# Optimization experiments

Hardware: AMD Instinct MI355X
Metric: run time of the kernel (lower is better)

The kernel has to match this reference:

```python
import jax, jax.numpy as jnp
import numpy as np

N_QUBITS = 10
DIM = 1 << N_QUBITS  # 1024

# Constant QFT matrix (PennyLane convention: F[j,k] = w^{jk}/sqrt(N), w = exp(2*pi*i/N),
# wire 0 = most significant bit). Symmetric, so state @ F == F @ state per sample.
_jk = (np.outer(np.arange(DIM), np.arange(DIM)) % DIM).astype(np.float64)
QFT_MAT = jnp.asarray((np.exp(2j * np.pi * _jk / DIM) / np.sqrt(DIM)).astype(np.complex64))


def _apply_1q(state, U, q):
    """Apply 2x2 gate U to wire q (wire 0 = MSB). state: [B, DIM] complex."""
    B = state.shape[0]
    left, right = 1 << q, 1 << (N_QUBITS - 1 - q)
    s = state.reshape(B, left, 2, right)
    s = jnp.einsum('ij,bajc->baic', U, s)
    return s.reshape(B, DIM)


def _apply_cnot(state, c, t):
    """CNOT with control c, target t (wire 0 = MSB)."""
    B = state.shape[0]
    a, b = (c, t) if c < t else (t, c)
    s = state.reshape(B, 1 << a, 2, 1 << (b - a - 1), 2, 1 << (N_QUBITS - 1 - b))
    ctrl_ax, tgt_ax = (2, 4) if c < t else (4, 2)
    s0 = jax.lax.index_in_dim(s, 0, ctrl_ax, keepdims=False)
    s1 = jax.lax.index_in_dim(s, 1, ctrl_ax, keepdims=False)
    ta = tgt_ax - 1 if tgt_ax > ctrl_ax else tgt_ax  # target axis after squeezing ctrl
    s1 = jnp.flip(s1, axis=ta)  # X on target when control == 1
    s = jnp.stack([s0, s1], axis=ctrl_ax)
    return s.reshape(B, DIM)


def _rx(t):
    c = jnp.cos(t / 2).astype(jnp.complex64)
    s = (-1j * jnp.sin(t / 2)).astype(jnp.complex64)
    return jnp.stack([jnp.stack([c, s]), jnp.stack([s, c])])


def _ry(t):
    c = jnp.cos(t / 2).astype(jnp.complex64)
    s = jnp.sin(t / 2).astype(jnp.complex64)
    return jnp.stack([jnp.stack([c, -s]), jnp.stack([s, c])])


def _rz(t):
    e = jnp.exp(-0.5j * t.astype(jnp.complex64))
    z = jnp.zeros((), jnp.complex64)
    return jnp.stack([jnp.stack([e, z]), jnp.stack([z, jnp.conj(e)])])


def _forward(x, weights):
    B = x.shape[0]
    # Pad/truncate is a no-op here (x already [B, DIM]); normalize as in the module.
    nrm = jnp.linalg.norm(x, axis=-1, keepdims=True)
    xn = x / jnp.maximum(nrm, 1e-8)
    state = xn.astype(jnp.complex64)  # AmplitudeEmbedding (already unit-norm)
    for q in range(N_QUBITS):
        state = _apply_1q(state, _rx(weights[q, 0]), q)
    for q in range(N_QUBITS):
        state = _apply_1q(state, _ry(weights[q, 1]), q)
    for q in range(N_QUBITS):
        state = _apply_1q(state, _rz(weights[q, 2]), q)
    for q in range(N_QUBITS):
        state = _apply_cnot(state, q, (q + 1) % N_QUBITS)
    for q in range(N_QUBITS):
        state = _apply_1q(state, _ry(weights[q, 3]), q)
    state = state @ QFT_MAT  # QFT (symmetric matrix)
    ex, ey, ez = [], [], []
    for q in range(N_QUBITS):
        s = state.reshape(B, 1 << q, 2, 1 << (N_QUBITS - 1 - q))
        s0, s1 = s[:, :, 0, :], s[:, :, 1, :]
        cross = jnp.sum(jnp.conj(s0) * s1, axis=(1, 2))
        ex.append(2.0 * jnp.real(cross))                # <X_q>
        ey.append(2.0 * jnp.imag(cross))                # <Y_q>
        ez.append(jnp.sum(jnp.abs(s0) ** 2 - jnp.abs(s1) ** 2, axis=(1, 2)))  # <Z_q>
    return jnp.stack(ex + ey + ez, axis=1).astype(jnp.float32)  # [B, 3*N_QUBITS]


def setup_inputs() -> dict:
    key = jax.random.key(0)
    kx, kw = jax.random.split(key)
    x = jax.random.normal(kx, (8192, 1024), dtype=jnp.float32)
    weights = jax.random.normal(kw, (10, 4), dtype=jnp.float32) * 0.01
    return {"x": x, "weights": weights}


def reference(x, weights):
    return _forward(x, weights)
```

## Files before the change

kernel.cpp:

```cpp
#include <hip/hip_runtime.h>


typedef _Float16 half8_t __attribute__((ext_vector_type(8)));
typedef _Float16 half4_t __attribute__((ext_vector_type(4)));
typedef float floatx4 __attribute__((ext_vector_type(4)));

#define GLB_CAST(p) ((const __attribute__((address_space(1))) void*)(p))
#define LDS_CAST(p) ((__attribute__((address_space(3))) void*)(p))

__global__ __launch_bounds__(256) void prep_kernel(const float* __restrict__ w,
                                                   const float* __restrict__ x,
                                                   _Float16* __restrict__ Wh,
                                                   _Float16* __restrict__ Xh)
{
    __shared__ float smem[2048 + 88];
    const int tid = threadIdx.x;

    if (blockIdx.x >= 1024) {
        float* wsum = smem;
        const int b = blockIdx.x - 1024;
        float4 v = ((const float4*)(x + (size_t)b * 1024))[tid];
        float ss = v.x*v.x + v.y*v.y + v.z*v.z + v.w*v.w;
        #pragma unroll
        for (int off = 32; off; off >>= 1) ss += __shfl_down(ss, off);
        if ((tid & 63) == 0) wsum[tid >> 6] = ss;
        __syncthreads();
        float scale = 1.0f / fmaxf(sqrtf(wsum[0] + wsum[1] + wsum[2] + wsum[3]), 1e-8f);
        half4_t h;
        h[0] = (_Float16)(v.x * scale);
        h[1] = (_Float16)(v.y * scale);
        h[2] = (_Float16)(v.z * scale);
        h[3] = (_Float16)(v.w * scale);
        ((half4_t*)(Xh + (size_t)b * 1024))[tid] = h;
        return;
    }

    float* sr  = smem;
    float* si  = smem + 1024;
    float* wc  = smem + 2048;
    float* wsn = smem + 2088;
    const int jb = blockIdx.x;

    if (tid < 40) {
        float t = w[tid] * 0.5f;
        wc[tid]  = cosf(t);
        wsn[tid] = sinf(t);
    }
    for (int i = tid; i < 1024; i += 256) { sr[i] = (i == jb) ? 1.0f : 0.0f; si[i] = 0.0f; }
    __syncthreads();

    for (int layer = 0; layer < 4; ++layer) {
        if (layer == 3) {
            for (int q = 0; q < 10; ++q) {
                int mc = 1 << (9 - q);
                int mt = 1 << (9 - ((q + 1) % 10));
                for (int p = tid; p < 512; p += 256) {
                    int i0 = ((p & ~(mt - 1)) << 1) | (p & (mt - 1));
                    if (i0 & mc) {
                        int i1 = i0 | mt;
                        float tr = sr[i0]; sr[i0] = sr[i1]; sr[i1] = tr;
                        float ti = si[i0]; si[i0] = si[i1]; si[i1] = ti;
                    }
                }
                __syncthreads();
            }
        }
        int wi = (layer == 3) ? 3 : layer;
        for (int q = 0; q < 10; ++q) {
            float c = wc[q * 4 + wi], s = wsn[q * 4 + wi];
            float u00r, u00i, u01r, u01i, u10r, u10i, u11r, u11i;
            if (layer == 0) {
                u00r=c; u00i=0; u01r=0; u01i=-s; u10r=0; u10i=-s; u11r=c; u11i=0;
            } else if (layer == 2) {
                u00r=c; u00i=-s; u01r=0; u01i=0; u10r=0; u10i=0; u11r=c; u11i=s;
            } else {
                u00r=c; u00i=0; u01r=-s; u01i=0; u10r=s; u10i=0; u11r=c; u11i=0;
            }
            int m = 1 << (9 - q);
            for (int p = tid; p < 512; p += 256) {
                int i0 = ((p & ~(m - 1)) << 1) | (p & (m - 1));
                int i1 = i0 | m;
                float ar = sr[i0], ai = si[i0], br = sr[i1], bi = si[i1];
                sr[i0] = u00r*ar - u00i*ai + u01r*br - u01i*bi;
                si[i0] = u00r*ai + u00i*ar + u01r*bi + u01i*br;
                sr[i1] = u10r*ar - u10i*ai + u11r*br - u11i*bi;
                si[i1] = u10r*ai + u10i*ar + u11r*bi + u11i*br;
            }
            __syncthreads();
        }
    }

    for (int i = tid; i < 1024; i += 256) {
        int r = (int)(__brev((unsigned)i) >> 22);
        if (r > i) {
            float tr = sr[i]; sr[i] = sr[r]; sr[r] = tr;
            float ti = si[i]; si[i] = si[r]; si[r] = ti;
        }
    }
    __syncthreads();
    for (int st = 1; st <= 10; ++st) {
        int hf = 1 << (st - 1);
        float astep = 6.28318530717958647f / (float)(1 << st);
        for (int p = tid; p < 512; p += 256) {
            int j2 = p & (hf - 1);
            int i0 = ((p >> (st - 1)) << st) | j2;
            int i1 = i0 + hf;
            float ang = astep * (float)j2;
            float sw, cw;
            __sincosf(ang, &sw, &cw);
            float br2 = sr[i1], bi2 = si[i1];
            float tr = cw*br2 - sw*bi2;
            float ti = cw*bi2 + sw*br2;
            float ur = sr[i0], ui = si[i0];
            sr[i0] = ur + tr; si[i0] = ui + ti;
            sr[i1] = ur - tr; si[i1] = ui - ti;
        }
        __syncthreads();
    }
    for (int k = tid; k < 1024; k += 256) {
        Wh[(size_t)jb * 2048 + 2*k]     = (_Float16)(sr[k] * 0.03125f);
        Wh[(size_t)jb * 2048 + 2*k + 1] = (_Float16)(si[k] * 0.03125f);
    }
}

__global__ __launch_bounds__(256) void transpose_kernel(const _Float16* __restrict__ Wh,
                                                        _Float16* __restrict__ Bt)
{
    __shared__ _Float16 tile[32][33];
    const int bx = blockIdx.x;
    const int by = blockIdx.y;
    const int tx = threadIdx.x;
    const int ty = threadIdx.y;
    #pragma unroll
    for (int i = 0; i < 4; ++i) {
        int r = ty + 8*i;
        tile[r][tx] = Wh[(size_t)(by*32 + r) * 2048 + bx*32 + tx];
    }
    __syncthreads();
    #pragma unroll
    for (int i = 0; i < 4; ++i) {
        int r = ty + 8*i;
        Bt[(size_t)(bx*32 + r) * 1024 + by*32 + tx] = tile[tx][r];
    }
}

__global__ __launch_bounds__(256, 2) void gemm_kernel(const _Float16* __restrict__ A,
                                                      const _Float16* __restrict__ Bt,
                                                      _Float16* __restrict__ C)
{
    __shared__ __align__(16) _Float16 As[128][64];
    __shared__ __align__(16) _Float16 Bs[128][64];
    const int tid  = threadIdx.x;
    const int wave = tid >> 6;
    const int lane = tid & 63;
    const int m0 = blockIdx.y * 128;
    const int n0 = blockIdx.x * 128;

    const int srow = lane >> 3;
    const int schk = (lane & 7) ^ srow;
    const _Float16* gA = A  + (size_t)(m0 + 32*wave + srow) * 1024 + schk * 8;
    const _Float16* gB = Bt + (size_t)(n0 + 32*wave + srow) * 1024 + schk * 8;
    _Float16* lA = &As[0][0] + wave*2048 + lane*8;
    _Float16* lB = &Bs[0][0] + wave*2048 + lane*8;

    const int fr = lane & 15;
    const int fc = lane >> 4;
    const int sx = fr & 7;
    const int wm = (wave >> 1) * 64;
    const int wn = (wave & 1) * 64;

    floatx4 acc[4][4];
    #pragma unroll
    for (int i = 0; i < 4; ++i)
        #pragma unroll
        for (int j = 0; j < 4; ++j)
            acc[i][j] = (floatx4){0.f, 0.f, 0.f, 0.f};

    for (int kt = 0; kt < 16; ++kt) {
        #pragma unroll
        for (int t = 0; t < 4; ++t) {
            __builtin_amdgcn_global_load_lds(GLB_CAST(gA + (size_t)t*8*1024), LDS_CAST(lA + t*512), 16, 0, 0);
            __builtin_amdgcn_global_load_lds(GLB_CAST(gB + (size_t)t*8*1024), LDS_CAST(lB + t*512), 16, 0, 0);
        }
        gA += 64; gB += 64;
        __syncthreads();
        #pragma unroll
        for (int kh = 0; kh < 2; ++kh) {
            half8_t af[4], bf[4];
            #pragma unroll
            for (int i = 0; i < 4; ++i)
                af[i] = *(const half8_t*)&As[wm + i*16 + fr][((kh*4 + fc) ^ sx) * 8];
            #pragma unroll
            for (int i = 0; i < 4; ++i)
                bf[i] = *(const half8_t*)&Bs[wn + i*16 + fr][((kh*4 + fc) ^ sx) * 8];
            #pragma unroll
            for (int mi = 0; mi < 4; ++mi)
                #pragma unroll
                for (int ni = 0; ni < 4; ++ni)
                    acc[mi][ni] = __builtin_amdgcn_mfma_f32_16x16x32_f16(af[mi], bf[ni], acc[mi][ni], 0, 0, 0);
        }
        __syncthreads();
    }

    #pragma unroll
    for (int mi = 0; mi < 4; ++mi) {
        #pragma unroll
        for (int r = 0; r < 4; ++r) {
            int row = m0 + wm + mi*16 + fc*4 + r;
            _Float16* cp = C + (size_t)row * 2048 + n0 + wn + fr;
            #pragma unroll
            for (int ni = 0; ni < 4; ++ni)
                cp[ni*16] = (_Float16)acc[mi][ni][r];
        }
    }
}

__device__ __forceinline__ float wred(float v) {
    v += __shfl_xor(v, 1);
    v += __shfl_xor(v, 2);
    v += __shfl_xor(v, 4);
    v += __shfl_xor(v, 8);
    v += __shfl_xor(v, 16);
    v += __shfl_xor(v, 32);
    return v;
}

__global__ __launch_bounds__(128, 2) void expect_kernel(const _Float16* __restrict__ Sh,
                                                        float* __restrict__ out)
{
    __shared__ __align__(16) float buf[2][2048];
    const int tid = threadIdx.x;
    const int w = tid >> 6, l = tid & 63;
    const int row = blockIdx.x * 2 + w;
    float* bw = buf[w];

    const _Float16* src = Sh + (size_t)row * 2048 + l * 32;
    float2 c[16];
    #pragma unroll
    for (int t = 0; t < 4; ++t) {
        half8_t v = ((const half8_t*)src)[t];
        #pragma unroll
        for (int u = 0; u < 4; ++u)
            c[t*4 + u] = make_float2((float)v[2*u], (float)v[2*u + 1]);
    }

    #pragma unroll
    for (int j = 0; j < 8; ++j) {
        int su = l*8 + (j ^ (l & 7));
        ((float4*)bw)[su] = make_float4(c[2*j].x, c[2*j].y, c[2*j+1].x, c[2*j+1].y);
    }

    float P2s = 0.f;
    #pragma unroll
    for (int i = 0; i < 16; ++i)
        P2s += c[i].x*c[i].x + c[i].y*c[i].y;

    float outv = 0.f;

    #pragma unroll
    for (int p = 0; p < 4; ++p) {
        const int m = 1 << p;
        const int q = 9 - p;
        float rr = 0.f, ii = 0.f, zz = 0.f;
        #pragma unroll
        for (int i = 0; i < 16; ++i) {
            if (i & m) continue;
            const int j = i | m;
            rr += c[i].x*c[j].x + c[i].y*c[j].y;
            ii += c[i].x*c[j].y - c[i].y*c[j].x;
            zz += (c[i].x*c[i].x + c[i].y*c[i].y) - (c[j].x*c[j].x + c[j].y*c[j].y);
        }
        rr = wred(rr);
        ii = wred(ii);
        zz = wred(zz);
        outv = (l == q)      ? 2.f*rr : outv;
        outv = (l == 10 + q) ? 2.f*ii : outv;
        outv = (l == 20 + q) ? zz     : outv;
    }

    #pragma unroll
    for (int e = 0; e < 6; ++e) {
        const int q = 5 - e;
        const int part = l ^ (1 << e);
        const int mybit = (l >> e) & 1;
        const float sgn = mybit ? -1.f : 1.f;
        const int j0 = mybit ? 4 : 0;
        float rr = 0.f, ii = 0.f;
        #pragma unroll
        for (int j = 0; j < 4; ++j) {
            const int su = part*8 + ((j0 + j) ^ (part & 7));
            float4 f = ((const float4*)bw)[su];
            const float2 a0 = c[2*j],     a1 = c[2*j + 1];
            const float2 b0 = c[2*j + 8], b1 = c[2*j + 9];
            const float m0x = mybit ? b0.x : a0.x;
            const float m0y = mybit ? b0.y : a0.y;
            const float m1x = mybit ? b1.x : a1.x;
            const float m1y = mybit ? b1.y : a1.y;
            rr += m0x*f.x + m0y*f.y;
            ii += m0x*f.y - m0y*f.x;
            rr += m1x*f.z + m1y*f.w;
            ii += m1x*f.w - m1y*f.z;
        }
        float rr_s = wred(rr);
        float ii_s = wred(sgn * ii);
        float zz_s = wred(sgn * P2s);
        outv = (l == q)      ? 2.f*rr_s : outv;
        outv = (l == 10 + q) ? 2.f*ii_s : outv;
        outv = (l == 20 + q) ? zz_s     : outv;
    }

    if (l < 30)
        out[(size_t)row * 30 + l] = outv;
}

extern "C" void kernel_launch(void* const* d_in, const int* in_sizes, int n_in,
                              void* d_out, int out_size, void* d_ws, size_t ws_size,
                              hipStream_t stream) {
    const float* x = (const float*)d_in[0];
    const float* w = (const float*)d_in[1];
    float* out = (float*)d_out;
    char* ws = (char*)d_ws;
    _Float16* Wh = (_Float16*)(ws);
    _Float16* Bt = (_Float16*)(ws + ((size_t)4  << 20));
    _Float16* Xh = (_Float16*)(ws + ((size_t)8  << 20));
    _Float16* Sh = (_Float16*)(ws + ((size_t)24 << 20));

    prep_kernel<<<9216, 256, 0, stream>>>(w, x, Wh, Xh);
    transpose_kernel<<<dim3(64, 32), dim3(32, 8), 0, stream>>>(Wh, Bt);
    gemm_kernel<<<dim3(16, 64), 256, 0, stream>>>(Xh, Bt, Sh);
    expect_kernel<<<4096, 128, 0, stream>>>(Sh, out);
}
```

Before: 172.1 us.

## Replace dense QFT GEMM pipeline with fused per-row gate simulation and FFT

Replaces the four-kernel pipeline (build a combined circuit matrix, transpose, fp16 MFMA GEMM, expectation) with a single kernel. Each wavefront loads one row and applies the fused RX·RY·RZ single-qubit gates, the CNOT ring as an index permutation through LDS, the RY layer and a radix-2 FFT for the QFT, all in registers with cross-lane shuffles. It then computes the expectation values. This drops the O(N^2) GEMM and its intermediate HBM traffic in favour of O(N log N) work per row. It also removes the fp16 quantisation, at the cost of many shuffles and sincos calls per element.

```diff
diff --git a/kernel.cpp b/kernel.cpp
--- a/kernel.cpp
+++ b/kernel.cpp
@@ -1,219 +1,5 @@
 #include <hip/hip_runtime.h>
 
-
-typedef _Float16 half8_t __attribute__((ext_vector_type(8)));
-typedef _Float16 half4_t __attribute__((ext_vector_type(4)));
-typedef float floatx4 __attribute__((ext_vector_type(4)));
-
-#define GLB_CAST(p) ((const __attribute__((address_space(1))) void*)(p))
-#define LDS_CAST(p) ((__attribute__((address_space(3))) void*)(p))
-
-__global__ __launch_bounds__(256) void prep_kernel(const float* __restrict__ w,
-                                                   const float* __restrict__ x,
-                                                   _Float16* __restrict__ Wh,
-                                                   _Float16* __restrict__ Xh)
-{
-    __shared__ float smem[2048 + 88];
-    const int tid = threadIdx.x;
-
-    if (blockIdx.x >= 1024) {
-        float* wsum = smem;
-        const int b = blockIdx.x - 1024;
-        float4 v = ((const float4*)(x + (size_t)b * 1024))[tid];
-        float ss = v.x*v.x + v.y*v.y + v.z*v.z + v.w*v.w;
-        #pragma unroll
-        for (int off = 32; off; off >>= 1) ss += __shfl_down(ss, off);
-        if ((tid & 63) == 0) wsum[tid >> 6] = ss;
-        __syncthreads();
-        float scale = 1.0f / fmaxf(sqrtf(wsum[0] + wsum[1] + wsum[2] + wsum[3]), 1e-8f);
-        half4_t h;
-        h[0] = (_Float16)(v.x * scale);
-        h[1] = (_Float16)(v.y * scale);
-        h[2] = (_Float16)(v.z * scale);
-        h[3] = (_Float16)(v.w * scale);
-        ((half4_t*)(Xh + (size_t)b * 1024))[tid] = h;
-        return;
-    }
-
-    float* sr  = smem;
-    float* si  = smem + 1024;
-    float* wc  = smem + 2048;
-    float* wsn = smem + 2088;
-    const int jb = blockIdx.x;
-
-    if (tid < 40) {
-        float t = w[tid] * 0.5f;
-        wc[tid]  = cosf(t);
-        wsn[tid] = sinf(t);
-    }
-    for (int i = tid; i < 1024; i += 256) { sr[i] = (i == jb) ? 1.0f : 0.0f; si[i] = 0.0f; }
-    __syncthreads();
-
-    for (int layer = 0; layer < 4; ++layer) {
-        if (layer == 3) {
-            for (int q = 0; q < 10; ++q) {
-                int mc = 1 << (9 - q);
-                int mt = 1 << (9 - ((q + 1) % 10));
-                for (int p = tid; p < 512; p += 256) {
-                    int i0 = ((p & ~(mt - 1)) << 1) | (p & (mt - 1));
-                    if (i0 & mc) {
-                        int i1 = i0 | mt;
-                        float tr = sr[i0]; sr[i0] = sr[i1]; sr[i1] = tr;
-                        float ti = si[i0]; si[i0] = si[i1]; si[i1] = ti;
-                    }
-                }
-                __syncthreads();
-            }
-        }
-        int wi = (layer == 3) ? 3 : layer;
-        for (int q = 0; q < 10; ++q) {
-            float c = wc[q * 4 + wi], s = wsn[q * 4 + wi];
-            float u00r, u00i, u01r, u01i, u10r, u10i, u11r, u11i;
-            if (layer == 0) {
-                u00r=c; u00i=0; u01r=0; u01i=-s; u10r=0; u10i=-s; u11r=c; u11i=0;
-            } else if (layer == 2) {
-                u00r=c; u00i=-s; u01r=0; u01i=0; u10r=0; u10i=0; u11r=c; u11i=s;
-            } else {
-                u00r=c; u00i=0; u01r=-s; u01i=0; u10r=s; u10i=0; u11r=c; u11i=0;
-            }
-            int m = 1 << (9 - q);
-            for (int p = tid; p < 512; p += 256) {
-                int i0 = ((p & ~(m - 1)) << 1) | (p & (m - 1));
-                int i1 = i0 | m;
-                float ar = sr[i0], ai = si[i0], br = sr[i1], bi = si[i1];
-                sr[i0] = u00r*ar - u00i*ai + u01r*br - u01i*bi;
-                si[i0] = u00r*ai + u00i*ar + u01r*bi + u01i*br;
-                sr[i1] = u10r*ar - u10i*ai + u11r*br - u11i*bi;
-                si[i1] = u10r*ai + u10i*ar + u11r*bi + u11i*br;
-            }
-            __syncthreads();
-        }
-    }
-
-    for (int i = tid; i < 1024; i += 256) {
-        int r = (int)(__brev((unsigned)i) >> 22);
-        if (r > i) {
-            float tr = sr[i]; sr[i] = sr[r]; sr[r] = tr;
-            float ti = si[i]; si[i] = si[r]; si[r] = ti;
-        }
-    }
-    __syncthreads();
-    for (int st = 1; st <= 10; ++st) {
-        int hf = 1 << (st - 1);
-        float astep = 6.28318530717958647f / (float)(1 << st);
-        for (int p = tid; p < 512; p += 256) {
-            int j2 = p & (hf - 1);
-            int i0 = ((p >> (st - 1)) << st) | j2;
-            int i1 = i0 + hf;
-            float ang = astep * (float)j2;
-            float sw, cw;
-            __sincosf(ang, &sw, &cw);
-            float br2 = sr[i1], bi2 = si[i1];
-            float tr = cw*br2 - sw*bi2;
-            float ti = cw*bi2 + sw*br2;
-            float ur = sr[i0], ui = si[i0];
-            sr[i0] = ur + tr; si[i0] = ui + ti;
-            sr[i1] = ur - tr; si[i1] = ui - ti;
-        }
-        __syncthreads();
-    }
-    for (int k = tid; k < 1024; k += 256) {
-        Wh[(size_t)jb * 2048 + 2*k]     = (_Float16)(sr[k] * 0.03125f);
-        Wh[(size_t)jb * 2048 + 2*k + 1] = (_Float16)(si[k] * 0.03125f);
-    }
-}
-
-__global__ __launch_bounds__(256) void transpose_kernel(const _Float16* __restrict__ Wh,
-                                                        _Float16* __restrict__ Bt)
-{
-    __shared__ _Float16 tile[32][33];
-    const int bx = blockIdx.x;
-    const int by = blockIdx.y;
-    const int tx = threadIdx.x;
-    const int ty = threadIdx.y;
-    #pragma unroll
-    for (int i = 0; i < 4; ++i) {
-        int r = ty + 8*i;
-        tile[r][tx] = Wh[(size_t)(by*32 + r) * 2048 + bx*32 + tx];
-    }
-    __syncthreads();
-    #pragma unroll
-    for (int i = 0; i < 4; ++i) {
-        int r = ty + 8*i;
-        Bt[(size_t)(bx*32 + r) * 1024 + by*32 + tx] = tile[tx][r];
-    }
-}
-
-__global__ __launch_bounds__(256, 2) void gemm_kernel(const _Float16* __restrict__ A,
-                                                      const _Float16* __restrict__ Bt,
-                                                      _Float16* __restrict__ C)
-{
-    __shared__ __align__(16) _Float16 As[128][64];
-    __shared__ __align__(16) _Float16 Bs[128][64];
-    const int tid  = threadIdx.x;
-    const int wave = tid >> 6;
-    const int lane = tid & 63;
-    const int m0 = blockIdx.y * 128;
-    const int n0 = blockIdx.x * 128;
-
-    const int srow = lane >> 3;
-    const int schk = (lane & 7) ^ srow;
-    const _Float16* gA = A  + (size_t)(m0 + 32*wave + srow) * 1024 + schk * 8;
-    const _Float16* gB = Bt + (size_t)(n0 + 32*wave + srow) * 1024 + schk * 8;
-    _Float16* lA = &As[0][0] + wave*2048 + lane*8;
-    _Float16* lB = &Bs[0][0] + wave*2048 + lane*8;
-
-    const int fr = lane & 15;
-    const int fc = lane >> 4;
-    const int sx = fr & 7;
-    const int wm = (wave >> 1) * 64;
-    const int wn = (wave & 1) * 64;
-
-    floatx4 acc[4][4];
-    #pragma unroll
-    for (int i = 0; i < 4; ++i)
-        #pragma unroll
-        for (int j = 0; j < 4; ++j)
-            acc[i][j] = (floatx4){0.f, 0.f, 0.f, 0.f};
-
-    for (int kt = 0; kt < 16; ++kt) {
-        #pragma unroll
-        for (int t = 0; t < 4; ++t) {
-            __builtin_amdgcn_global_load_lds(GLB_CAST(gA + (size_t)t*8*1024), LDS_CAST(lA + t*512), 16, 0, 0);
-            __builtin_amdgcn_global_load_lds(GLB_CAST(gB + (size_t)t*8*1024), LDS_CAST(lB + t*512), 16, 0, 0);
-        }
-        gA += 64; gB += 64;
-        __syncthreads();
-        #pragma unroll
-        for (int kh = 0; kh < 2; ++kh) {
-            half8_t af[4], bf[4];
-            #pragma unroll
-            for (int i = 0; i < 4; ++i)
-                af[i] = *(const half8_t*)&As[wm + i*16 + fr][((kh*4 + fc) ^ sx) * 8];
-            #pragma unroll
-            for (int i = 0; i < 4; ++i)
-                bf[i] = *(const half8_t*)&Bs[wn + i*16 + fr][((kh*4 + fc) ^ sx) * 8];
-            #pragma unroll
-            for (int mi = 0; mi < 4; ++mi)
-                #pragma unroll
-                for (int ni = 0; ni < 4; ++ni)
-                    acc[mi][ni] = __builtin_amdgcn_mfma_f32_16x16x32_f16(af[mi], bf[ni], acc[mi][ni], 0, 0, 0);
-        }
-        __syncthreads();
-    }
-
-    #pragma unroll
-    for (int mi = 0; mi < 4; ++mi) {
-        #pragma unroll
-        for (int r = 0; r < 4; ++r) {
-            int row = m0 + wm + mi*16 + fc*4 + r;
-            _Float16* cp = C + (size_t)row * 2048 + n0 + wn + fr;
-            #pragma unroll
-            for (int ni = 0; ni < 4; ++ni)
-                cp[ni*16] = (_Float16)acc[mi][ni][r];
-        }
-    }
-}
 
 __device__ __forceinline__ float wred(float v) {
     v += __shfl_xor(v, 1);
@@ -225,28 +11,186 @@
     return v;
 }
 
-__global__ __launch_bounds__(128, 2) void expect_kernel(const _Float16* __restrict__ Sh,
-                                                        float* __restrict__ out)
+__global__ __launch_bounds__(256) void fused_kernel(const float* __restrict__ w,
+                                                    const float* __restrict__ x,
+                                                    float* __restrict__ out)
 {
-    __shared__ __align__(16) float buf[2][2048];
+    __shared__ float uu[10][8];
+    __shared__ float ryc[10], rys[10];
+    __shared__ __align__(16) float scr[4][2048];
     const int tid = threadIdx.x;
-    const int w = tid >> 6, l = tid & 63;
-    const int row = blockIdx.x * 2 + w;
-    float* bw = buf[w];
-
-    const _Float16* src = Sh + (size_t)row * 2048 + l * 32;
+    const int wv = tid >> 6, l = tid & 63;
+    const int row = blockIdx.x * 4 + wv;
+    float* bw = scr[wv];
+
+    if (tid < 10) {
+        float t0 = w[tid*4 + 0] * 0.5f, t1 = w[tid*4 + 1] * 0.5f;
+        float t2 = w[tid*4 + 2] * 0.5f, t3 = w[tid*4 + 3] * 0.5f;
+        float s0, c0, s1, c1, s2, c2, s3, c3;
+        __sincosf(t0, &s0, &c0);
+        __sincosf(t1, &s1, &c1);
+        __sincosf(t2, &s2, &c2);
+        __sincosf(t3, &s3, &c3);
+        uu[tid][0] =  c2*c1*c0 + s2*s1*s0;
+        uu[tid][1] =  c2*s1*s0 - s2*c1*c0;
+        uu[tid][2] = -(c2*s1*c0 + s2*c1*s0);
+        uu[tid][3] =  s2*s1*c0 - c2*c1*s0;
+        uu[tid][4] =  c2*s1*c0 + s2*c1*s0;
+        uu[tid][5] =  s2*s1*c0 - c2*c1*s0;
+        uu[tid][6] =  c2*c1*c0 + s2*s1*s0;
+        uu[tid][7] =  s2*c1*c0 - c2*s1*s0;
+        ryc[tid] = c3;
+        rys[tid] = s3;
+    }
+    __syncthreads();
+
+    const float* xr = x + (size_t)row * 1024 + l * 16;
+    float4 v0 = ((const float4*)xr)[0];
+    float4 v1 = ((const float4*)xr)[1];
+    float4 v2 = ((const float4*)xr)[2];
+    float4 v3 = ((const float4*)xr)[3];
+    float ss = v0.x*v0.x + v0.y*v0.y + v0.z*v0.z + v0.w*v0.w
+             + v1.x*v1.x + v1.y*v1.y + v1.z*v1.z + v1.w*v1.w
+             + v2.x*v2.x + v2.y*v2.y + v2.z*v2.z + v2.w*v2.w
+             + v3.x*v3.x + v3.y*v3.y + v3.z*v3.z + v3.w*v3.w;
+    ss = wred(ss);
+    const float scale = 0.03125f / fmaxf(sqrtf(ss), 1e-8f);
+
     float2 c[16];
-    #pragma unroll
-    for (int t = 0; t < 4; ++t) {
-        half8_t v = ((const half8_t*)src)[t];
-        #pragma unroll
-        for (int u = 0; u < 4; ++u)
-            c[t*4 + u] = make_float2((float)v[2*u], (float)v[2*u + 1]);
+    c[0]  = make_float2(v0.x*scale, 0.f); c[1]  = make_float2(v0.y*scale, 0.f);
+    c[2]  = make_float2(v0.z*scale, 0.f); c[3]  = make_float2(v0.w*scale, 0.f);
+    c[4]  = make_float2(v1.x*scale, 0.f); c[5]  = make_float2(v1.y*scale, 0.f);
+    c[6]  = make_float2(v1.z*scale, 0.f); c[7]  = make_float2(v1.w*scale, 0.f);
+    c[8]  = make_float2(v2.x*scale, 0.f); c[9]  = make_float2(v2.y*scale, 0.f);
+    c[10] = make_float2(v2.z*scale, 0.f); c[11] = make_float2(v2.w*scale, 0.f);
+    c[12] = make_float2(v3.x*scale, 0.f); c[13] = make_float2(v3.y*scale, 0.f);
+    c[14] = make_float2(v3.z*scale, 0.f); c[15] = make_float2(v3.w*scale, 0.f);
+
+    #pragma unroll
+    for (int p = 0; p < 4; ++p) {
+        const float* U = uu[9 - p];
+        const float u00r = U[0], u00i = U[1], u01r = U[2], u01i = U[3];
+        const float u10r = U[4], u10i = U[5], u11r = U[6], u11i = U[7];
+        const int m = 1 << p;
+        #pragma unroll
+        for (int i = 0; i < 16; ++i) {
+            if (i & m) continue;
+            const int j = i | m;
+            const float ar = c[i].x, ai = c[i].y, br = c[j].x, bi = c[j].y;
+            c[i].x = u00r*ar - u00i*ai + u01r*br - u01i*bi;
+            c[i].y = u00r*ai + u00i*ar + u01r*bi + u01i*br;
+            c[j].x = u10r*ar - u10i*ai + u11r*br - u11i*bi;
+            c[j].y = u10r*ai + u10i*ar + u11r*bi + u11i*br;
+        }
+    }
+    #pragma unroll
+    for (int e = 0; e < 6; ++e) {
+        const float* U = uu[5 - e];
+        const int mybit = (l >> e) & 1;
+        const float car = mybit ? U[6] : U[0];
+        const float cai = mybit ? U[7] : U[1];
+        const float cbr = mybit ? U[4] : U[2];
+        const float cbi = mybit ? U[5] : U[3];
+        #pragma unroll
+        for (int i = 0; i < 16; ++i) {
+            const float fr = __shfl_xor(c[i].x, 1 << e);
+            const float fi = __shfl_xor(c[i].y, 1 << e);
+            const float ar = c[i].x, ai = c[i].y;
+            c[i].x = car*ar - cai*ai + cbr*fr - cbi*fi;
+            c[i].y = car*ai + cai*ar + cbr*fi + cbi*fr;
+        }
     }
 
     #pragma unroll
     for (int j = 0; j < 8; ++j) {
-        int su = l*8 + (j ^ (l & 7));
+        const int su = l*8 + (j ^ (l & 7));
+        ((float4*)bw)[su] = make_float4(c[2*j].x, c[2*j].y, c[2*j+1].x, c[2*j+1].y);
+    }
+    #pragma unroll
+    for (int i = 0; i < 16; ++i) {
+        const int k = l*16 + i;
+        int m = (int)(__brev((unsigned)k) >> 22);
+        #pragma unroll
+        for (int q = 9; q >= 0; --q) {
+            const int pc = (q == 9) ? 0 : 9 - q;
+            const int pt = (q == 9) ? 9 : 8 - q;
+            m ^= ((m >> pc) & 1) << pt;
+        }
+        const int lm = m >> 4, um = (m >> 1) & 7, lo = m & 1;
+        const int su = lm*8 + (um ^ (lm & 7));
+        c[i] = ((const float2*)bw)[su*2 + lo];
+    }
+
+    #pragma unroll
+    for (int p = 0; p < 4; ++p) {
+        const float cc = ryc[p], sv = rys[p];
+        const int m = 1 << p;
+        #pragma unroll
+        for (int i = 0; i < 16; ++i) {
+            if (i & m) continue;
+            const int j = i | m;
+            const float ar = c[i].x, ai = c[i].y, br = c[j].x, bi = c[j].y;
+            c[i].x = cc*ar - sv*br;  c[i].y = cc*ai - sv*bi;
+            c[j].x = sv*ar + cc*br;  c[j].y = sv*ai + cc*bi;
+        }
+    }
+    #pragma unroll
+    for (int e = 0; e < 6; ++e) {
+        const float cc = ryc[4 + e], sv = rys[4 + e];
+        const int mybit = (l >> e) & 1;
+        const float sel = mybit ? sv : -sv;
+        #pragma unroll
+        for (int i = 0; i < 16; ++i) {
+            const float fr = __shfl_xor(c[i].x, 1 << e);
+            const float fi = __shfl_xor(c[i].y, 1 << e);
+            c[i].x = cc*c[i].x + sel*fr;
+            c[i].y = cc*c[i].y + sel*fi;
+        }
+    }
+
+    #pragma unroll
+    for (int st = 1; st <= 4; ++st) {
+        const int hf = 1 << (st - 1);
+        const float astep = 6.28318530717958647f / (float)(1 << st);
+        #pragma unroll
+        for (int i = 0; i < 16; ++i) {
+            if (i & hf) continue;
+            const int j = i | hf;
+            float sw, cw;
+            __sincosf(astep * (float)(i & (hf - 1)), &sw, &cw);
+            const float tr = cw*c[j].x - sw*c[j].y;
+            const float ti = cw*c[j].y + sw*c[j].x;
+            const float ur = c[i].x, ui = c[i].y;
+            c[i].x = ur + tr; c[i].y = ui + ti;
+            c[j].x = ur - tr; c[j].y = ui - ti;
+        }
+    }
+    #pragma unroll
+    for (int e2 = 0; e2 < 6; ++e2) {
+        const int st = 5 + e2;
+        const float astep = 6.28318530717958647f / (float)(1 << st);
+        const int mybit = (l >> e2) & 1;
+        const float base = astep * 16.0f * (float)(l & ((1 << e2) - 1));
+        #pragma unroll
+        for (int i = 0; i < 16; ++i) {
+            const float fr = __shfl_xor(c[i].x, 1 << e2);
+            const float fi = __shfl_xor(c[i].y, 1 << e2);
+            float sw, cw;
+            __sincosf(base + astep * (float)i, &sw, &cw);
+            const float zr = mybit ? c[i].x : fr;
+            const float zi = mybit ? c[i].y : fi;
+            const float tr = cw*zr - sw*zi;
+            const float ti = cw*zi + sw*zr;
+            const float ur = mybit ? fr : c[i].x;
+            const float ui = mybit ? fi : c[i].y;
+            c[i].x = mybit ? (ur - tr) : (ur + tr);
+            c[i].y = mybit ? (ui - ti) : (ui + ti);
+        }
+    }
+
+    #pragma unroll
+    for (int j = 0; j < 8; ++j) {
+        const int su = l*8 + (j ^ (l & 7));
         ((float4*)bw)[su] = make_float4(c[2*j].x, c[2*j].y, c[2*j+1].x, c[2*j+1].y);
     }
 
@@ -289,7 +233,7 @@
         #pragma unroll
         for (int j = 0; j < 4; ++j) {
             const int su = part*8 + ((j0 + j) ^ (part & 7));
-            float4 f = ((const float4*)bw)[su];
+            const float4 f = ((const float4*)bw)[su];
             const float2 a0 = c[2*j],     a1 = c[2*j + 1];
             const float2 b0 = c[2*j + 8], b1 = c[2*j + 9];
             const float m0x = mybit ? b0.x : a0.x;
@@ -301,9 +245,9 @@
             rr += m1x*f.z + m1y*f.w;
             ii += m1x*f.w - m1y*f.z;
         }
-        float rr_s = wred(rr);
-        float ii_s = wred(sgn * ii);
-        float zz_s = wred(sgn * P2s);
+        const float rr_s = wred(rr);
+        const float ii_s = wred(sgn * ii);
+        const float zz_s = wred(sgn * P2s);
         outv = (l == q)      ? 2.f*rr_s : outv;
         outv = (l == 10 + q) ? 2.f*ii_s : outv;
         outv = (l == 20 + q) ? zz_s     : outv;
@@ -319,14 +263,7 @@
     const float* x = (const float*)d_in[0];
     const float* w = (const float*)d_in[1];
     float* out = (float*)d_out;
-    char* ws = (char*)d_ws;
-    _Float16* Wh = (_Float16*)(ws);
-    _Float16* Bt = (_Float16*)(ws + ((size_t)4  << 20));
-    _Float16* Xh = (_Float16*)(ws + ((size_t)8  << 20));
-    _Float16* Sh = (_Float16*)(ws + ((size_t)24 << 20));
-
-    prep_kernel<<<9216, 256, 0, stream>>>(w, x, Wh, Xh);
-    transpose_kernel<<<dim3(64, 32), dim3(32, 8), 0, stream>>>(Wh, Bt);
-    gemm_kernel<<<dim3(16, 64), 256, 0, stream>>>(Xh, Bt, Sh);
-    expect_kernel<<<4096, 128, 0, stream>>>(Sh, out);
+    (void)d_ws; (void)ws_size;
+
+    fused_kernel<<<2048, 256, 0, stream>>>(w, x, out);
 }
```

Measured after the change: 157.9 us. 1.09x faster.
